# Optimization experiments

Hardware: AMD Instinct MI355X
Metric: run time of the kernel (lower is better)

Reference implementation:

```python
import jax, jax.numpy as jnp
import numpy as np

B, S, D = 2, 2048, 1024
H, HK, HD = 16, 4, 64          # query heads, kv heads, head dim = D//H
WIN = 1024                     # sliding attention window
E, K, DH = 8, 2, 2048          # experts, top_k, expert hidden (== d_head ctor arg)
ATTN_EPS, FFN_EPS = 1e-5, 1e-6
ROPE_THETA = 10000.0


def setup_inputs() -> dict:
    key = jax.random.key(0)
    ks = jax.random.split(key, 9)
    sc = 0.02
    # real rotary frequencies for positions [start_pos, start_pos+S)
    start_pos = 0
    inv_freq = 1.0 / (ROPE_THETA ** (jnp.arange(0, HD, 2, dtype=jnp.float32) / HD))  # [HD//2]
    pos = jnp.arange(start_pos, start_pos + S, dtype=jnp.float32)
    ang = pos[:, None] * inv_freq[None, :]  # [S, HD//2]
    return {
        'x': jax.random.normal(ks[0], (B, S, D), jnp.float32),
        'freqs_cos': jnp.cos(ang),
        'freqs_sin': jnp.sin(ang),
        'attn_norm_w': jnp.ones((D,), jnp.float32),
        'wq': jax.random.normal(ks[1], (D, H * HD), jnp.float32) * sc,
        'wk': jax.random.normal(ks[2], (D, HK * HD), jnp.float32) * sc,
        'wv': jax.random.normal(ks[3], (D, HK * HD), jnp.float32) * sc,
        'wo': jax.random.normal(ks[4], (H * HD, D), jnp.float32) * sc,
        'ffn_norm_w': jnp.ones((D,), jnp.float32),
        'router_w': jax.random.normal(ks[5], (D, E), jnp.float32) * sc,
        'w1': jax.random.normal(ks[6], (E, D, DH), jnp.float32) * sc,
        'w2': jax.random.normal(ks[7], (E, DH, D), jnp.float32) * sc,
        'start_pos': start_pos,
    }


def _rmsnorm(x, w, eps):
    return x * jax.lax.rsqrt(jnp.mean(x * x, axis=-1, keepdims=True) + eps) * w


def _rope(t, cos, sin):
    # t: [B,S,N,HD]; cos/sin: [S,HD//2] -> complex rotation on consecutive pairs
    shp = t.shape
    t = t.reshape(shp[:-1] + (HD // 2, 2))
    t0, t1 = t[..., 0], t[..., 1]
    c = cos[None, :, None, :]
    s = sin[None, :, None, :]
    r = jnp.stack([t0 * c - t1 * s, t0 * s + t1 * c], axis=-1)
    return r.reshape(shp)


def reference(x, freqs_cos, freqs_sin, attn_norm_w, wq, wk, wv, wo,
              ffn_norm_w, router_w, w1, w2, start_pos):
    # ---- attention sublayer (RMSNorm -> GQA sliding-window attn) ----
    hn = _rmsnorm(x, attn_norm_w, ATTN_EPS)
    q = (hn @ wq).reshape(B, S, H, HD)
    k = (hn @ wk).reshape(B, S, HK, HD)
    v = (hn @ wv).reshape(B, S, HK, HD)
    q = _rope(q, freqs_cos, freqs_sin)
    k = _rope(k, freqs_cos, freqs_sin)
    rep = H // HK
    k = jnp.repeat(k, rep, axis=2)  # [B,S,H,HD]
    v = jnp.repeat(v, rep, axis=2)
    scale = 1.0 / np.sqrt(HD).astype(np.float32)
    scores = jnp.einsum('bqhd,bkhd->bhqk', q, k) * scale  # [B,H,S,S]
    qi = jnp.arange(S) + start_pos
    kj = jnp.arange(S) + start_pos
    mask = (kj[None, :] <= qi[:, None]) & (qi[:, None] - kj[None, :] < WIN)
    scores = jnp.where(mask[None, None], scores, jnp.float32(-1e30))
    attn = jax.nn.softmax(scores, axis=-1)
    o = jnp.einsum('bhqk,bkhd->bqhd', attn, v).reshape(B, S, H * HD)
    h = x + o @ wo

    # ---- MoE sublayer (RMSNorm -> router top-k -> expert FFNs) ----
    fn = _rmsnorm(h, ffn_norm_w, FFN_EPS).reshape(-1, D)  # [T,D], T=B*S
    probs = jax.nn.softmax(fn @ router_w, axis=-1)        # [T,E]
    top_vals, top_idx = jax.lax.top_k(probs, K)           # [T,K]
    gates = top_vals / jnp.sum(top_vals, axis=-1, keepdims=True)
    gmat = jnp.sum(jax.nn.one_hot(top_idx, E, dtype=fn.dtype) * gates[..., None], axis=1)  # [T,E]
    moe = jnp.zeros_like(fn)
    for e in range(E):  # fixed small expert count
        moe = moe + gmat[:, e:e + 1] * (jax.nn.silu(fn @ w1[e]) @ w2[e])
    return h + moe.reshape(B, S, D)
```

## Files before the change

kernel.cpp:

```cpp
#include <hip/hip_runtime.h>
#include <hip/hip_bf16.h>

using bf16 = __hip_bfloat16;
typedef __attribute__((ext_vector_type(8))) short bf16x8;
typedef __attribute__((ext_vector_type(4))) short short4v;
typedef __attribute__((ext_vector_type(4))) float f32x4;

#define DEV static __device__ __forceinline__

DEV float b2f(bf16 v) { return __bfloat162float(v); }
DEV bf16  f2b(float f) { return __float2bfloat16(f); }
DEV short bbits(float f) { bf16 h = __float2bfloat16(f); short u; __builtin_memcpy(&u, &h, 2); return u; }
DEV float sb2f(short s) {
  unsigned u = ((unsigned)(unsigned short)s) << 16;
  float f; __builtin_memcpy(&f, &u, 4); return f;
}

#define GL2LDS(g, l)                                                        \
  __builtin_amdgcn_global_load_lds(                                         \
      (const __attribute__((address_space(1))) void*)(g),                   \
      (__attribute__((address_space(3))) void*)(l), 16, 0, 0)

__global__ __launch_bounds__(256) void transpose_convert(
    const float* __restrict__ src, bf16* __restrict__ dst, int K, int N) {
  __shared__ float tile[64][65];
  int n0 = blockIdx.x * 64, k0 = blockIdx.y * 64;
  src += (size_t)blockIdx.z * K * N;
  dst += (size_t)blockIdx.z * K * N;
  int t = threadIdx.x;
  int rr = t >> 4, cc = (t & 15) * 4;
#pragma unroll
  for (int p = 0; p < 4; ++p) {
    int r = rr + p * 16;
    const float4 v = *(const float4*)&src[(size_t)(k0 + r) * N + n0 + cc];
    tile[r][cc] = v.x; tile[r][cc + 1] = v.y; tile[r][cc + 2] = v.z; tile[r][cc + 3] = v.w;
  }
  __syncthreads();
#pragma unroll
  for (int p = 0; p < 4; ++p) {
    int nr = rr + p * 16;
    short4v o;
    o[0] = bbits(tile[cc + 0][nr]);
    o[1] = bbits(tile[cc + 1][nr]);
    o[2] = bbits(tile[cc + 2][nr]);
    o[3] = bbits(tile[cc + 3][nr]);
    *(short4v*)&dst[(size_t)(n0 + nr) * K + k0 + cc] = o;
  }
}

__global__ __launch_bounds__(256) void rmsnorm_kernel(
    const float* __restrict__ x, const float* __restrict__ w,
    bf16* __restrict__ o, float eps) {
  int row = blockIdx.x;
  const float* xr = x + (size_t)row * 1024;
  int t = threadIdx.x;
  float4 v = *(const float4*)&xr[t * 4];
  float ss = v.x * v.x + v.y * v.y + v.z * v.z + v.w * v.w;
#pragma unroll
  for (int d = 32; d; d >>= 1) ss += __shfl_down(ss, d);
  __shared__ float red[4];
  if ((t & 63) == 0) red[t >> 6] = ss;
  __syncthreads();
  float sum = red[0] + red[1] + red[2] + red[3];
  float sc = rsqrtf(sum * (1.f / 1024.f) + eps);
  const float4 wv = *(const float4*)&w[t * 4];
  short4v pk;
  pk[0] = bbits(v.x * sc * wv.x);
  pk[1] = bbits(v.y * sc * wv.y);
  pk[2] = bbits(v.z * sc * wv.z);
  pk[3] = bbits(v.w * sc * wv.w);
  *(short4v*)&o[(size_t)row * 1024 + t * 4] = pk;
}

__global__ __launch_bounds__(256) void rmsnorm_router(
    const float* __restrict__ h, const float* __restrict__ w,
    const float* __restrict__ rw, bf16* __restrict__ fn,
    float* __restrict__ gates, int* __restrict__ eidx) {
  int row = blockIdx.x;
  const float* hr = h + (size_t)row * 1024;
  int t = threadIdx.x;
  float4 v = *(const float4*)&hr[t * 4];
  float ss = v.x * v.x + v.y * v.y + v.z * v.z + v.w * v.w;
#pragma unroll
  for (int d = 32; d; d >>= 1) ss += __shfl_down(ss, d);
  __shared__ float red[4];
  __shared__ float red2[4][8];
  if ((t & 63) == 0) red[t >> 6] = ss;
  __syncthreads();
  float sum = red[0] + red[1] + red[2] + red[3];
  float sc = rsqrtf(sum * (1.f / 1024.f) + 1e-6f);
  const float4 wv = *(const float4*)&w[t * 4];
  float f0 = v.x * sc * wv.x, f1 = v.y * sc * wv.y;
  float f2 = v.z * sc * wv.z, f3 = v.w * sc * wv.w;
  short4v pk;
  pk[0] = bbits(f0); pk[1] = bbits(f1); pk[2] = bbits(f2); pk[3] = bbits(f3);
  *(short4v*)&fn[(size_t)row * 1024 + t * 4] = pk;
  const float* rr = rw + (size_t)t * 4 * 8;
  float lg[8];
#pragma unroll
  for (int e = 0; e < 8; ++e)
    lg[e] = f0 * rr[e] + f1 * rr[8 + e] + f2 * rr[16 + e] + f3 * rr[24 + e];
#pragma unroll
  for (int d = 32; d; d >>= 1)
#pragma unroll
    for (int e = 0; e < 8; ++e) lg[e] += __shfl_down(lg[e], d);
  if ((t & 63) == 0)
#pragma unroll
    for (int e = 0; e < 8; ++e) red2[t >> 6][e] = lg[e];
  __syncthreads();
  if (t == 0) {
    float L[8];
#pragma unroll
    for (int e = 0; e < 8; ++e)
      L[e] = red2[0][e] + red2[1][e] + red2[2][e] + red2[3][e];
    int e0 = 0; float v0 = L[0];
#pragma unroll
    for (int e = 1; e < 8; ++e) if (L[e] > v0) { v0 = L[e]; e0 = e; }
    int e1 = -1; float v1 = -1e30f;
#pragma unroll
    for (int e = 0; e < 8; ++e) if (e != e0 && L[e] > v1) { v1 = L[e]; e1 = e; }
    float r1 = expf(v1 - v0);
    float den = 1.f + r1;
    gates[row * 2] = 1.f / den;
    gates[row * 2 + 1] = r1 / den;
    eidx[row * 2] = e0;
    eidx[row * 2 + 1] = e1;
  }
}

__global__ __launch_bounds__(256) void rope_all(
    bf16* __restrict__ qb, bf16* __restrict__ kbuf,
    const float* __restrict__ fcos, const float* __restrict__ fsin) {
  int tid = blockIdx.x * 256 + threadIdx.x;
  bf16* p; int srow, i;
  if (tid < 2097152) {
    int row = tid >> 9, cp = tid & 511;
    p = qb + (size_t)row * 1024 + cp * 2;
    srow = row & 2047; i = cp & 31;
  } else {
    int t2 = tid - 2097152;
    int row = t2 >> 7, cp = t2 & 127;
    p = kbuf + (size_t)row * 256 + cp * 2;
    srow = row & 2047; i = cp & 31;
  }
  float t0 = b2f(p[0]), t1 = b2f(p[1]);
  float c = fcos[srow * 32 + i], sn = fsin[srow * 32 + i];
  p[0] = f2b(t0 * c - t1 * sn);
  p[1] = f2b(t0 * sn + t1 * c);
}

template <int MODE>
__global__ __launch_bounds__(256) void gemm_bt(
    const bf16* __restrict__ A, const bf16* __restrict__ Bt,
    int M, int N, int Kd,
    bf16* __restrict__ outb, bf16* __restrict__ outk, bf16* __restrict__ outv,
    float* __restrict__ outf, const float* __restrict__ resid,
    const int* __restrict__ counts, const int* __restrict__ offsets,
    const int* __restrict__ tok, const float* __restrict__ gatel) {
  int count = M, off = 0;
  const bf16* Ap = A;
  const bf16* Bp = Bt;
  int mb, nb;
  if (MODE == 2 || MODE == 3) {
    int e = blockIdx.y;
    count = counts[e]; off = offsets[e];
    Bp = Bt + (size_t)e * Kd * N;
    if (MODE == 3) Ap = A + (size_t)off * Kd;
    mb = blockIdx.z * 128; nb = blockIdx.x * 128;
  } else {
    int gx = gridDim.x;
    int flat = blockIdx.y * gx + blockIdx.x;
    int cpx = (gx * gridDim.y) >> 3;
    int swz = (flat & 7) * cpx + (flat >> 3);
    mb = (swz / gx) * 128; nb = (swz % gx) * 128;
  }
  if (mb >= count) return;

  __shared__ __align__(16) bf16 As[2][128 * 32];
  __shared__ __align__(16) bf16 Bs[2][128 * 32];

  int t = threadIdx.x;
  int lane = t & 63, wid = t >> 6;

  const bf16* agl[2];
  const bf16* bgl[2];
#pragma unroll
  for (int iss = 0; iss < 2; ++iss) {
    int p = iss * 256 + wid * 64 + lane;
    int row = p >> 2, cs = p & 3;
    int c = cs ^ (row & 3);
    int m = mb + row;
    const bf16* abase;
    if (MODE == 2) {
      int tokid = (m < count) ? tok[off + m] : 0;
      abase = A + (size_t)tokid * Kd;
    } else {
      int mm = (m < count) ? m : 0;
      abase = Ap + (size_t)mm * Kd;
    }
    agl[iss] = abase + c * 8;
    bgl[iss] = Bp + (size_t)(nb + row) * Kd + c * 8;
  }

  int wr = (wid >> 1) * 64, wc = (wid & 1) * 64;
  int lr = lane & 15, lkc = lane >> 4;

  auto stage = [&](int buf, int kt) {
#pragma unroll
    for (int iss = 0; iss < 2; ++iss) {
      GL2LDS(agl[iss] + kt * 32, &As[buf][(iss * 256 + wid * 64) * 8]);
      GL2LDS(bgl[iss] + kt * 32, &Bs[buf][(iss * 256 + wid * 64) * 8]);
    }
  };

  const f32x4 fzero = {0.f, 0.f, 0.f, 0.f};
  f32x4 acc[4][4];
#pragma unroll
  for (int i = 0; i < 4; ++i)
#pragma unroll
    for (int j = 0; j < 4; ++j) acc[i][j] = fzero;

  int nk = Kd >> 5;
  stage(0, 0);
  __syncthreads();
  for (int kt = 0; kt < nk; ++kt) {
    int cur = kt & 1;
    if (kt + 1 < nk) stage(cur ^ 1, kt + 1);
    bf16x8 af[4], bfr[4];
#pragma unroll
    for (int i = 0; i < 4; ++i) {
      int r = wr + i * 16 + lr;
      af[i] = *(const bf16x8*)&As[cur][r * 32 + ((lkc ^ (r & 3)) * 8)];
    }
#pragma unroll
    for (int j = 0; j < 4; ++j) {
      int r = wc + j * 16 + lr;
      bfr[j] = *(const bf16x8*)&Bs[cur][r * 32 + ((lkc ^ (r & 3)) * 8)];
    }
#pragma unroll
    for (int i = 0; i < 4; ++i)
#pragma unroll
      for (int j = 0; j < 4; ++j)
        acc[i][j] = __builtin_amdgcn_mfma_f32_16x16x32_bf16(af[i], bfr[j], acc[i][j], 0, 0, 0);
    __syncthreads();
  }

  int rq = lane >> 4;
#pragma unroll
  for (int i = 0; i < 4; ++i) {
#pragma unroll
    for (int j = 0; j < 4; ++j) {
      if (MODE == 5) {
        int n = nb + wc + j * 16 + lr;
        if (n >= 1280) {
          int vcol = n - 1280;
          int kh = vcol >> 6, d = vcol & 63;
          int m0 = mb + wr + i * 16 + rq * 4;
          int bb = m0 >> 11, s = m0 & 2047;
          short4v pk;
#pragma unroll
          for (int r = 0; r < 4; ++r) pk[r] = bbits(acc[i][j][r]);
          *(short4v*)&outv[((size_t)((bb * 4 + kh) * 64 + d)) * 2048 + s] = pk;
        } else {
#pragma unroll
          for (int r = 0; r < 4; ++r) {
            int m = mb + wr + i * 16 + rq * 4 + r;
            float v = acc[i][j][r];
            if (n < 1024) outb[(size_t)m * 1024 + n] = f2b(v);
            else          outk[(size_t)m * 256 + (n - 1024)] = f2b(v);
          }
        }
      } else {
#pragma unroll
        for (int r = 0; r < 4; ++r) {
          int m = mb + wr + i * 16 + rq * 4 + r;
          int n = nb + wc + j * 16 + lr;
          float v = acc[i][j][r];
          if (MODE == 1) {
            outf[(size_t)m * N + n] = resid[(size_t)m * N + n] + v;
          } else if (MODE == 2) {
            if (m < count) {
              float sg = 1.f / (1.f + expf(-v));
              outb[(size_t)(off + m) * N + n] = f2b(v * sg);
            }
          } else if (MODE == 3) {
            if (m < count) {
              int row = off + m;
              outb[(size_t)row * N + n] = f2b(gatel[row] * v);
            }
          }
        }
      }
    }
  }
}

__global__ __launch_bounds__(256) void attn_kernel(
    const bf16* __restrict__ q, const bf16* __restrict__ kb,
    const bf16* __restrict__ vt, bf16* __restrict__ o) {
  int qb = blockIdx.x, h = blockIdx.y, b = blockIdx.z;
  int kh = h >> 2;
  int t = threadIdx.x;
  int lane = t & 63, wid = t >> 6;
  int lr = lane & 15, lkc = lane >> 4;
  int q0 = qb * 64;
  int qrow = q0 + wid * 16;

  __shared__ __align__(16) bf16 Ks[64 * 64];
  __shared__ __align__(16) bf16 Vs[64 * 64];
  __shared__ __align__(16) bf16 Ps[4][16 * 72];

  bf16x8 aq[2];
#pragma unroll
  for (int kk = 0; kk < 2; ++kk)
    aq[kk] = *(const bf16x8*)&q[(size_t)(b * 2048 + qrow + lr) * 1024 + h * 64 + kk * 32 + lkc * 8];

  const f32x4 fzero = {0.f, 0.f, 0.f, 0.f};
  f32x4 oacc[4];
  float mrun[4], lrun[4];
#pragma unroll
  for (int r = 0; r < 4; ++r) { oacc[r] = fzero; mrun[r] = -1e30f; lrun[r] = 0.f; }

  int klo = q0 - 1023; if (klo < 0) klo = 0;
  int tlo = klo >> 6, thi = q0 >> 6;
  int skey = t >> 3;
  int sch = t & 7;

  for (int kt = tlo; kt <= thi; ++kt) {
    int kbase = kt * 64;
#pragma unroll
    for (int pp = 0; pp < 2; ++pp) {
      int key = skey + pp * 32;
      bf16x8 kv = *(const bf16x8*)&kb[(size_t)(b * 2048 + kbase + key) * 256 + kh * 64 + sch * 8];
      *(bf16x8*)&Ks[key * 64 + ((sch ^ (key & 7)) * 8)] = kv;
      bf16x8 vv = *(const bf16x8*)&vt[((size_t)((b * 4 + kh) * 64 + key)) * 2048 + kbase + sch * 8];
      *(bf16x8*)&Vs[key * 64 + ((sch ^ (key & 7)) * 8)] = vv;
    }
    __syncthreads();

    f32x4 sacc[4];
#pragma unroll
    for (int nt = 0; nt < 4; ++nt) sacc[nt] = fzero;
#pragma unroll
    for (int nt = 0; nt < 4; ++nt)
#pragma unroll
      for (int kk = 0; kk < 2; ++kk) {
        int r = nt * 16 + lr;
        bf16x8 bk = *(const bf16x8*)&Ks[r * 64 + (((kk * 4 + lkc) ^ (r & 7)) * 8)];
        sacc[nt] = __builtin_amdgcn_mfma_f32_16x16x32_bf16(aq[kk], bk, sacc[nt], 0, 0, 0);
      }

    float sval[4][4], mt[4];
    int qg = qrow + lkc * 4;
#pragma unroll
    for (int r = 0; r < 4; ++r) mt[r] = -1e30f;
#pragma unroll
    for (int nt = 0; nt < 4; ++nt) {
      int kkey = kbase + nt * 16 + lr;
#pragma unroll
      for (int r = 0; r < 4; ++r) {
        float s = sacc[nt][r] * 0.125f;
        int qq = qg + r;
        bool valid = (kkey <= qq) && (qq - kkey < 1024);
        s = valid ? s : -1e30f;
        sval[nt][r] = s;
        mt[r] = fmaxf(mt[r], s);
      }
    }
#pragma unroll
    for (int d = 1; d < 16; d <<= 1)
#pragma unroll
      for (int r = 0; r < 4; ++r) mt[r] = fmaxf(mt[r], __shfl_xor(mt[r], d));
    float alpha[4], rs[4];
#pragma unroll
    for (int r = 0; r < 4; ++r) {
      float mn = fmaxf(mrun[r], mt[r]);
      alpha[r] = __expf(mrun[r] - mn);
      mrun[r] = mn;
      rs[r] = 0.f;
    }
#pragma unroll
    for (int nt = 0; nt < 4; ++nt)
#pragma unroll
      for (int r = 0; r < 4; ++r) {
        float pv = __expf(sval[nt][r] - mrun[r]);
        sval[nt][r] = pv;
        rs[r] += pv;
      }
#pragma unroll
    for (int d = 1; d < 16; d <<= 1)
#pragma unroll
      for (int r = 0; r < 4; ++r) rs[r] += __shfl_xor(rs[r], d);
#pragma unroll
    for (int r = 0; r < 4; ++r) lrun[r] = lrun[r] * alpha[r] + rs[r];
#pragma unroll
    for (int dt = 0; dt < 4; ++dt) {
      f32x4 t4 = oacc[dt];
#pragma unroll
      for (int r = 0; r < 4; ++r) t4[r] *= alpha[r];
      oacc[dt] = t4;
    }

    bf16* pw = &Ps[wid][0];
#pragma unroll
    for (int nt = 0; nt < 4; ++nt)
#pragma unroll
      for (int r = 0; r < 4; ++r)
        pw[(lkc * 4 + r) * 72 + nt * 16 + lr] = f2b(sval[nt][r]);
    __syncthreads();

    bf16x8 pa[2];
#pragma unroll
    for (int kk2 = 0; kk2 < 2; ++kk2)
      pa[kk2] = *(const bf16x8*)&pw[lr * 72 + kk2 * 32 + lkc * 8];
#pragma unroll
    for (int dt = 0; dt < 4; ++dt)
#pragma unroll
      for (int kk2 = 0; kk2 < 2; ++kk2) {
        int rrow = dt * 16 + lr;
        bf16x8 bv = *(const bf16x8*)&Vs[rrow * 64 + (((kk2 * 4 + lkc) ^ (rrow & 7)) * 8)];
        oacc[dt] = __builtin_amdgcn_mfma_f32_16x16x32_bf16(pa[kk2], bv, oacc[dt], 0, 0, 0);
      }
    __syncthreads();
  }

#pragma unroll
  for (int dt = 0; dt < 4; ++dt)
#pragma unroll
    for (int r = 0; r < 4; ++r) {
      int qq = qrow + lkc * 4 + r;
      int dd = dt * 16 + lr;
      o[(size_t)(b * 2048 + qq) * 1024 + h * 64 + dd] = f2b(oacc[dt][r] / lrun[r]);
    }
}

__global__ __launch_bounds__(1024) void moe_setup(
    const int* __restrict__ eidx, const float* __restrict__ gates,
    int* __restrict__ counts, int* __restrict__ offsets,
    int* __restrict__ tok, float* __restrict__ gatel, int* __restrict__ inv) {
  __shared__ int hist[8];
  __shared__ int cur[8];
  int t = threadIdx.x;
  if (t < 8) hist[t] = 0;
  __syncthreads();
  int e[8];
#pragma unroll
  for (int c = 0; c < 8; ++c) {
    e[c] = eidx[c * 1024 + t];
    atomicAdd(&hist[e[c]], 1);
  }
  __syncthreads();
  if (t == 0) {
    int o = 0;
#pragma unroll
    for (int i = 0; i < 8; ++i) {
      offsets[i] = o; cur[i] = o;
      int cnt = hist[i]; counts[i] = cnt; o += cnt;
    }
  }
  __syncthreads();
#pragma unroll
  for (int c = 0; c < 8; ++c) {
    int i = c * 1024 + t;
    int pos = atomicAdd(&cur[e[c]], 1);
    tok[pos] = i >> 1;
    gatel[pos] = gates[i];
    inv[i] = pos;
  }
}

__global__ __launch_bounds__(256) void final_add(
    const float* __restrict__ h, const bf16* __restrict__ y2,
    const int* __restrict__ inv, float* __restrict__ out) {
  int tokid = blockIdx.x;
  int t = threadIdx.x;
  int i0 = inv[tokid * 2], i1 = inv[tokid * 2 + 1];
  size_t base = (size_t)tokid * 1024 + t * 4;
  float4 a = *(const float4*)&h[base];
  short4v p0 = *(const short4v*)&y2[(size_t)i0 * 1024 + t * 4];
  short4v p1 = *(const short4v*)&y2[(size_t)i1 * 1024 + t * 4];
  float4 o;
  o.x = a.x + sb2f(p0[0]) + sb2f(p1[0]);
  o.y = a.y + sb2f(p0[1]) + sb2f(p1[1]);
  o.z = a.z + sb2f(p0[2]) + sb2f(p1[2]);
  o.w = a.w + sb2f(p0[3]) + sb2f(p1[3]);
  *(float4*)&out[base] = o;
}

extern "C" void kernel_launch(void* const* d_in, const int* in_sizes, int n_in,
                              void* d_out, int out_size, void* d_ws, size_t ws_size,
                              hipStream_t stream) {
  const float* x    = (const float*)d_in[0];
  const float* fcos = (const float*)d_in[1];
  const float* fsin = (const float*)d_in[2];
  const float* attw = (const float*)d_in[3];
  const float* wq   = (const float*)d_in[4];
  const float* wk   = (const float*)d_in[5];
  const float* wv   = (const float*)d_in[6];
  const float* wo   = (const float*)d_in[7];
  const float* ffnw = (const float*)d_in[8];
  const float* rw   = (const float*)d_in[9];
  const float* w1   = (const float*)d_in[10];
  const float* w2   = (const float*)d_in[11];
  float* out = (float*)d_out;

  const int M = 4096;
  char* p = (char*)d_ws;
  auto alloc = [&](size_t b) { char* r = p; p += (b + 255) & ~(size_t)255; return r; };

  bf16* hn     = (bf16*)alloc((size_t)M * 1024 * 2);
  bf16* qb     = (bf16*)alloc((size_t)M * 1024 * 2);
  bf16* kbuf   = (bf16*)alloc((size_t)M * 256 * 2);
  bf16* vt     = (bf16*)alloc((size_t)M * 256 * 2);
  bf16* ob     = (bf16*)alloc((size_t)M * 1024 * 2);
  float* hbuf  = (float*)alloc((size_t)M * 1024 * 4);
  bf16* fn     = (bf16*)alloc((size_t)M * 1024 * 2);
  bf16* wqkvt  = (bf16*)alloc((size_t)1536 * 1024 * 2);
  bf16* wot    = (bf16*)alloc((size_t)1024 * 1024 * 2);
  bf16* w1t    = (bf16*)alloc((size_t)8 * 2048 * 1024 * 2);
  bf16* w2t    = (bf16*)alloc((size_t)8 * 1024 * 2048 * 2);
  bf16* act    = (bf16*)alloc((size_t)8192 * 2048 * 2);
  bf16* y2     = (bf16*)alloc((size_t)8192 * 1024 * 2);
  float* gates = (float*)alloc((size_t)M * 2 * 4);
  int* eidx    = (int*)alloc((size_t)M * 2 * 4);
  int* counts  = (int*)alloc(8 * 4);
  int* offsets = (int*)alloc(8 * 4);
  int* tok     = (int*)alloc(8192 * 4);
  int* inv     = (int*)alloc(8192 * 4);
  float* gatel = (float*)alloc(8192 * 4);

  transpose_convert<<<dim3(16, 16, 1), 256, 0, stream>>>(wq, wqkvt, 1024, 1024);
  transpose_convert<<<dim3(4, 16, 1), 256, 0, stream>>>(wk, wqkvt + (size_t)1024 * 1024, 1024, 256);
  transpose_convert<<<dim3(4, 16, 1), 256, 0, stream>>>(wv, wqkvt + (size_t)1280 * 1024, 1024, 256);
  transpose_convert<<<dim3(16, 16, 1), 256, 0, stream>>>(wo, wot, 1024, 1024);
  transpose_convert<<<dim3(32, 16, 8), 256, 0, stream>>>(w1, w1t, 1024, 2048);
  transpose_convert<<<dim3(16, 32, 8), 256, 0, stream>>>(w2, w2t, 2048, 1024);

  rmsnorm_kernel<<<M, 256, 0, stream>>>(x, attw, hn, 1e-5f);

  gemm_bt<5><<<dim3(12, 32, 1), 256, 0, stream>>>(hn, wqkvt, M, 1536, 1024,
      qb, kbuf, vt, nullptr, nullptr, nullptr, nullptr, nullptr, nullptr);

  rope_all<<<10240, 256, 0, stream>>>(qb, kbuf, fcos, fsin);

  attn_kernel<<<dim3(32, 16, 2), 256, 0, stream>>>(qb, kbuf, vt, ob);

  gemm_bt<1><<<dim3(8, 32, 1), 256, 0, stream>>>(ob, wot, M, 1024, 1024,
      nullptr, nullptr, nullptr, hbuf, x, nullptr, nullptr, nullptr, nullptr);

  rmsnorm_router<<<M, 256, 0, stream>>>(hbuf, ffnw, rw, fn, gates, eidx);
  moe_setup<<<1, 1024, 0, stream>>>(eidx, gates, counts, offsets, tok, gatel, inv);

  gemm_bt<2><<<dim3(16, 8, 64), 256, 0, stream>>>(fn, w1t, M, 2048, 1024,
      act, nullptr, nullptr, nullptr, nullptr, counts, offsets, tok, nullptr);
  gemm_bt<3><<<dim3(8, 8, 64), 256, 0, stream>>>(act, w2t, M, 1024, 2048,
      y2, nullptr, nullptr, nullptr, nullptr, counts, offsets, tok, gatel);

  final_add<<<M, 256, 0, stream>>>(hbuf, y2, inv, out);
}
```

Measured before the change: 350.6 us.

## Fuse RoPE into QKV GEMM epilogue and double GEMM K-tile to 64

Removes the standalone rope_all kernel and applies the rotary rotation in the QKV GEMM epilogue, pairing adjacent columns through a lane shuffle. This avoids an extra read-modify-write pass over Q and K. Separately, every gemm_bt instance now stages a K-tile of 64 instead of 32, with an 8-way XOR swizzle in LDS. The larger tile halves the number of barrier iterations but doubles shared memory per block, which may reduce occupancy.

```diff
diff --git a/kernel.cpp b/kernel.cpp
--- a/kernel.cpp
+++ b/kernel.cpp
@@ -128,33 +128,13 @@
   }
 }
 
-__global__ __launch_bounds__(256) void rope_all(
-    bf16* __restrict__ qb, bf16* __restrict__ kbuf,
-    const float* __restrict__ fcos, const float* __restrict__ fsin) {
-  int tid = blockIdx.x * 256 + threadIdx.x;
-  bf16* p; int srow, i;
-  if (tid < 2097152) {
-    int row = tid >> 9, cp = tid & 511;
-    p = qb + (size_t)row * 1024 + cp * 2;
-    srow = row & 2047; i = cp & 31;
-  } else {
-    int t2 = tid - 2097152;
-    int row = t2 >> 7, cp = t2 & 127;
-    p = kbuf + (size_t)row * 256 + cp * 2;
-    srow = row & 2047; i = cp & 31;
-  }
-  float t0 = b2f(p[0]), t1 = b2f(p[1]);
-  float c = fcos[srow * 32 + i], sn = fsin[srow * 32 + i];
-  p[0] = f2b(t0 * c - t1 * sn);
-  p[1] = f2b(t0 * sn + t1 * c);
-}
-
 template <int MODE>
 __global__ __launch_bounds__(256) void gemm_bt(
     const bf16* __restrict__ A, const bf16* __restrict__ Bt,
     int M, int N, int Kd,
     bf16* __restrict__ outb, bf16* __restrict__ outk, bf16* __restrict__ outv,
     float* __restrict__ outf, const float* __restrict__ resid,
+    const float* __restrict__ fcos, const float* __restrict__ fsin,
     const int* __restrict__ counts, const int* __restrict__ offsets,
     const int* __restrict__ tok, const float* __restrict__ gatel) {
   int count = M, off = 0;
@@ -176,19 +156,19 @@
   }
   if (mb >= count) return;
 
-  __shared__ __align__(16) bf16 As[2][128 * 32];
-  __shared__ __align__(16) bf16 Bs[2][128 * 32];
+  __shared__ __align__(16) bf16 As[2][128 * 64];
+  __shared__ __align__(16) bf16 Bs[2][128 * 64];
 
   int t = threadIdx.x;
   int lane = t & 63, wid = t >> 6;
 
-  const bf16* agl[2];
-  const bf16* bgl[2];
-#pragma unroll
-  for (int iss = 0; iss < 2; ++iss) {
-    int p = iss * 256 + wid * 64 + lane;
-    int row = p >> 2, cs = p & 3;
-    int c = cs ^ (row & 3);
+  const bf16* agl[4];
+  const bf16* bgl[4];
+#pragma unroll
+  for (int l = 0; l < 4; ++l) {
+    int c = l * 256 + t;
+    int row = c >> 3, slot = c & 7;
+    int kc = slot ^ (row & 7);
     int m = mb + row;
     const bf16* abase;
     if (MODE == 2) {
@@ -198,8 +178,8 @@
       int mm = (m < count) ? m : 0;
       abase = Ap + (size_t)mm * Kd;
     }
-    agl[iss] = abase + c * 8;
-    bgl[iss] = Bp + (size_t)(nb + row) * Kd + c * 8;
+    agl[l] = abase + kc * 8;
+    bgl[l] = Bp + (size_t)(nb + row) * Kd + kc * 8;
   }
 
   int wr = (wid >> 1) * 64, wc = (wid & 1) * 64;
@@ -207,9 +187,9 @@
 
   auto stage = [&](int buf, int kt) {
 #pragma unroll
-    for (int iss = 0; iss < 2; ++iss) {
-      GL2LDS(agl[iss] + kt * 32, &As[buf][(iss * 256 + wid * 64) * 8]);
-      GL2LDS(bgl[iss] + kt * 32, &Bs[buf][(iss * 256 + wid * 64) * 8]);
+    for (int l = 0; l < 4; ++l) {
+      GL2LDS(agl[l] + kt * 64, &As[buf][(l * 256 + t) * 8]);
+      GL2LDS(bgl[l] + kt * 64, &Bs[buf][(l * 256 + t) * 8]);
     }
   };
 
@@ -220,28 +200,31 @@
 #pragma unroll
     for (int j = 0; j < 4; ++j) acc[i][j] = fzero;
 
-  int nk = Kd >> 5;
+  int nk = Kd >> 6;
   stage(0, 0);
   __syncthreads();
   for (int kt = 0; kt < nk; ++kt) {
     int cur = kt & 1;
     if (kt + 1 < nk) stage(cur ^ 1, kt + 1);
-    bf16x8 af[4], bfr[4];
-#pragma unroll
-    for (int i = 0; i < 4; ++i) {
-      int r = wr + i * 16 + lr;
-      af[i] = *(const bf16x8*)&As[cur][r * 32 + ((lkc ^ (r & 3)) * 8)];
-    }
-#pragma unroll
-    for (int j = 0; j < 4; ++j) {
-      int r = wc + j * 16 + lr;
-      bfr[j] = *(const bf16x8*)&Bs[cur][r * 32 + ((lkc ^ (r & 3)) * 8)];
-    }
-#pragma unroll
-    for (int i = 0; i < 4; ++i)
-#pragma unroll
-      for (int j = 0; j < 4; ++j)
-        acc[i][j] = __builtin_amdgcn_mfma_f32_16x16x32_bf16(af[i], bfr[j], acc[i][j], 0, 0, 0);
+#pragma unroll
+    for (int kk = 0; kk < 2; ++kk) {
+      bf16x8 af[4], bfr[4];
+#pragma unroll
+      for (int i = 0; i < 4; ++i) {
+        int r = wr + i * 16 + lr;
+        af[i] = *(const bf16x8*)&As[cur][r * 64 + (((kk * 4 + lkc) ^ (r & 7)) * 8)];
+      }
+#pragma unroll
+      for (int j = 0; j < 4; ++j) {
+        int r = wc + j * 16 + lr;
+        bfr[j] = *(const bf16x8*)&Bs[cur][r * 64 + (((kk * 4 + lkc) ^ (r & 7)) * 8)];
+      }
+#pragma unroll
+      for (int i = 0; i < 4; ++i)
+#pragma unroll
+        for (int j = 0; j < 4; ++j)
+          acc[i][j] = __builtin_amdgcn_mfma_f32_16x16x32_bf16(af[i], bfr[j], acc[i][j], 0, 0, 0);
+    }
     __syncthreads();
   }
 
@@ -262,12 +245,18 @@
           for (int r = 0; r < 4; ++r) pk[r] = bbits(acc[i][j][r]);
           *(short4v*)&outv[((size_t)((bb * 4 + kh) * 64 + d)) * 2048 + s] = pk;
         } else {
+          int ii = (n & 63) >> 1;
+          bool odd = n & 1;
 #pragma unroll
           for (int r = 0; r < 4; ++r) {
             int m = mb + wr + i * 16 + rq * 4 + r;
+            int s = m & 2047;
             float v = acc[i][j][r];
-            if (n < 1024) outb[(size_t)m * 1024 + n] = f2b(v);
-            else          outk[(size_t)m * 256 + (n - 1024)] = f2b(v);
+            float vp = __shfl_xor(v, 1);
+            float c = fcos[s * 32 + ii], sn = fsin[s * 32 + ii];
+            float o = odd ? (vp * sn + v * c) : (v * c - vp * sn);
+            if (n < 1024) outb[(size_t)m * 1024 + n] = f2b(o);
+            else          outk[(size_t)m * 256 + (n - 1024)] = f2b(o);
           }
         }
       } else {
@@ -539,22 +528,20 @@
   rmsnorm_kernel<<<M, 256, 0, stream>>>(x, attw, hn, 1e-5f);
 
   gemm_bt<5><<<dim3(12, 32, 1), 256, 0, stream>>>(hn, wqkvt, M, 1536, 1024,
-      qb, kbuf, vt, nullptr, nullptr, nullptr, nullptr, nullptr, nullptr);
-
-  rope_all<<<10240, 256, 0, stream>>>(qb, kbuf, fcos, fsin);
+      qb, kbuf, vt, nullptr, nullptr, fcos, fsin, nullptr, nullptr, nullptr, nullptr);
 
   attn_kernel<<<dim3(32, 16, 2), 256, 0, stream>>>(qb, kbuf, vt, ob);
 
   gemm_bt<1><<<dim3(8, 32, 1), 256, 0, stream>>>(ob, wot, M, 1024, 1024,
-      nullptr, nullptr, nullptr, hbuf, x, nullptr, nullptr, nullptr, nullptr);
+      nullptr, nullptr, nullptr, hbuf, x, nullptr, nullptr, nullptr, nullptr, nullptr, nullptr);
 
   rmsnorm_router<<<M, 256, 0, stream>>>(hbuf, ffnw, rw, fn, gates, eidx);
   moe_setup<<<1, 1024, 0, stream>>>(eidx, gates, counts, offsets, tok, gatel, inv);
 
   gemm_bt<2><<<dim3(16, 8, 64), 256, 0, stream>>>(fn, w1t, M, 2048, 1024,
-      act, nullptr, nullptr, nullptr, nullptr, counts, offsets, tok, nullptr);
+      act, nullptr, nullptr, nullptr, nullptr, nullptr, nullptr, counts, offsets, tok, nullptr);
   gemm_bt<3><<<dim3(8, 8, 64), 256, 0, stream>>>(act, w2t, M, 1024, 2048,
-      y2, nullptr, nullptr, nullptr, nullptr, counts, offsets, tok, gatel);
+      y2, nullptr, nullptr, nullptr, nullptr, nullptr, nullptr, counts, offsets, tok, gatel);
 
   final_add<<<M, 256, 0, stream>>>(hbuf, y2, inv, out);
 }
```

Measured after the change: 372.0 us. +6.1%, slower.
